# Optimization experiments

Measured on AMD Instinct MI355X. Metric: run time of the kernel, lower is better.

Reference implementation:

```python
import jax, jax.numpy as jnp
import numpy as np

B, S, N, SD = 1024, 8, 64, 36
EPS = 1e-5

def _lrelu(x):
    return jnp.where(x > 0, x, 0.01 * x)

def _inorm(x, g, b):
    # x: [B,S,N,C]; InstanceNorm(axis=3) on a [1,1,N,C] tensor normalizes over N per channel
    mu = jnp.mean(x, axis=2, keepdims=True)
    var = jnp.var(x, axis=2, keepdims=True)
    return (x - mu) * jax.lax.rsqrt(var + EPS) * g + b

def _conv1d_same(x, w, b):
    # x: [B,S,Cin], w: [K,Cin,Cout]; TF 'same' even-kernel pads (0, k-1-pl)
    k = w.shape[0]
    pl = (k - 1) // 2
    y = jax.lax.conv_general_dilated(x, w, (1,), [(pl, k - 1 - pl)],
                                     dimension_numbers=('NWC', 'WIO', 'NWC'))
    return y + b

def setup_inputs() -> dict:
    key = jax.random.key(0)
    ks = iter(jax.random.split(key, 64))
    d = {}
    d['fts'] = jax.random.normal(next(ks), (B, S, N, 5), jnp.float32)
    d['state'] = jax.random.normal(next(ks), (B, S, SD), jnp.float32)
    def w(shape, scale=0.05):
        return jax.random.normal(next(ks), shape, jnp.float32) * scale
    # pointnet (1x1 Conv2D == pointwise matmul)
    d['pw1'] = w((5, 32)); d['pb1'] = jnp.zeros((32,)); d['pg1'] = jnp.ones((32,)); d['pbe1'] = jnp.zeros((32,))
    d['pw2'] = w((32, 64)); d['pb2'] = jnp.zeros((64,)); d['pg2'] = jnp.ones((64,)); d['pbe2'] = jnp.zeros((64,))
    d['pw3'] = w((64, 128)); d['pb3'] = jnp.zeros((128,)); d['pg3'] = jnp.ones((128,)); d['pbe3'] = jnp.zeros((128,))
    d['pw4'] = w((128, 128)); d['pb4'] = jnp.zeros((128,))
    # fts_mergenet Conv1D stack + Dense
    d['mw1'] = w((2, 128, 128)); d['mb1'] = jnp.zeros((128,))
    d['mw2'] = w((2, 128, 64)); d['mb2'] = jnp.zeros((64,))
    d['mw3'] = w((2, 64, 64)); d['mb3'] = jnp.zeros((64,))
    d['mw4'] = w((2, 64, 64)); d['mb4'] = jnp.zeros((64,))
    d['mdw'] = w((S * 64, 128)); d['mdb'] = jnp.zeros((128,))
    # states_conv Conv1D stack + Dense
    d['sw1'] = w((2, SD, 128)); d['sb1'] = jnp.zeros((128,))
    d['sw2'] = w((2, 128, 64)); d['sb2'] = jnp.zeros((64,))
    d['sw3'] = w((2, 64, 64)); d['sb3'] = jnp.zeros((64,))
    d['sw4'] = w((2, 64, 64)); d['sb4'] = jnp.zeros((64,))
    d['sdw'] = w((S * 64, 128)); d['sdb'] = jnp.zeros((128,))
    # control module Dense stack
    d['cw1'] = w((256, 128)); d['cb1'] = jnp.zeros((128,))
    d['cw2'] = w((128, 64)); d['cb2'] = jnp.zeros((64,))
    d['cw3'] = w((64, 32)); d['cb3'] = jnp.zeros((32,))
    d['cw4'] = w((32, 4)); d['cb4'] = jnp.zeros((4,))
    return d

def reference(fts, state, pw1, pb1, pg1, pbe1, pw2, pb2, pg2, pbe2,
              pw3, pb3, pg3, pbe3, pw4, pb4,
              mw1, mb1, mw2, mb2, mw3, mb3, mw4, mb4, mdw, mdb,
              sw1, sb1, sw2, sb2, sw3, sb3, sw4, sb4, sdw, sdb,
              cw1, cb1, cw2, cb2, cw3, cb3, cw4, cb4):
    # --- pointnet, fully batched over (B,S) instead of tf.map_fn per timestep ---
    x = fts  # [B,S,N,5]
    x = _lrelu(_inorm(jnp.einsum('bsnc,cd->bsnd', x, pw1) + pb1, pg1, pbe1))
    x = _lrelu(_inorm(jnp.einsum('bsnc,cd->bsnd', x, pw2) + pb2, pg2, pbe2))
    x = _lrelu(_inorm(jnp.einsum('bsnc,cd->bsnd', x, pw3) + pb3, pg3, pbe3))
    x = jnp.einsum('bsnc,cd->bsnd', x, pw4) + pb4
    emb = jnp.mean(x, axis=2)  # GlobalAveragePooling2D over (1,N) -> [B,S,128]
    # --- fts_mergenet ---
    y = _lrelu(_conv1d_same(emb, mw1, mb1))
    y = _lrelu(_conv1d_same(y, mw2, mb2))
    y = _lrelu(_conv1d_same(y, mw3, mb3))
    y = _lrelu(_conv1d_same(y, mw4, mb4))
    fts_emb = y.reshape(y.shape[0], -1) @ mdw + mdb  # [B,128]
    # --- states branch ---
    z = _lrelu(_conv1d_same(state, sw1, sb1))
    z = _lrelu(_conv1d_same(z, sw2, sb2))
    z = _lrelu(_conv1d_same(z, sw3, sb3))
    z = _conv1d_same(z, sw4, sb4)  # no activation after 4th conv
    st_emb = z.reshape(z.shape[0], -1) @ sdw + sdb  # [B,128]
    # --- control head ---
    t = jnp.concatenate([fts_emb, st_emb], axis=1)  # [B,256]
    t = _lrelu(t @ cw1 + cb1)
    t = _lrelu(t @ cw2 + cb2)
    t = _lrelu(t @ cw3 + cb3)
    out = t @ cw4 + cb4  # [B,4]
    thrust = jax.nn.sigmoid(out[:, :1])
    body = jnp.tanh(out[:, 1:])
    mult = jnp.array([21.0, 6.0, 6.0, 6.0], dtype=out.dtype)
    return jnp.concatenate([thrust, body], axis=1) * mult
```

## Files before the change

### kernel.cpp

```cpp
#include <hip/hip_runtime.h>
#include <math.h>

#define THREADS 256

constexpr int S   = 8;
constexpr int NPT = 64;
constexpr int SD  = 36;
constexpr float EPS = 1e-5f;

typedef float v4f __attribute__((ext_vector_type(4)));
typedef __attribute__((ext_vector_type(8))) short bf8;
typedef __attribute__((ext_vector_type(4))) float f4;

__device__ __forceinline__ float lrelu(float x) { return x > 0.f ? x : 0.01f * x; }

__device__ __forceinline__ unsigned short f2bf(float x) {
  union { float f; unsigned u; } v; v.f = x;
  unsigned r = v.u + 0x7FFFu + ((v.u >> 16) & 1u);
  return (unsigned short)(r >> 16);
}

__device__ __forceinline__ void pack_frag(const float* __restrict__ src, unsigned short* __restrict__ dst,
                                          int slot, int NT, int TS, int CIN, int N) {
  const int f = slot >> 6, l = slot & 63;
  const int nt = f % NT, kt = f / NT;
  const int n = nt * 16 + (l & 15), g = (l >> 4);
  unsigned short* d = dst + (size_t)f * 512 + l * 8;
#pragma unroll
  for (int j = 0; j < 8; ++j) {
    int k = kt * 32 + g * 8 + j;
    float v;
    if (TS > 0) { int tap = k / TS, c = k - tap * TS; v = (c < CIN) ? src[(tap * CIN + c) * N + n] : 0.f; }
    else        v = (CIN == 0 || k < CIN) ? src[k * N + n] : 0.f;
    d[j] = f2bf(v);
  }
}

#define WOFF_PNW1 0
#define WOFF_PNW2 1024
#define WOFF_PNW3 3072
#define WOFF_MW1  11264
#define WOFF_MW2  44032
#define WOFF_MW3  60416
#define WOFF_MW4  68608
#define WOFF_MDW  76800
#define WOFF_SW1  142336
#define WOFF_SW2  154624
#define WOFF_SW3  171008
#define WOFF_SW4  179200
#define WOFF_SDW  187392

__global__ __launch_bounds__(THREADS)
void fold_kernel(const float* __restrict__ pw4, const float* __restrict__ pb4,
                 const float* __restrict__ mw1, const float* __restrict__ mb1,
                 float* __restrict__ w1f, float* __restrict__ mb1p, float* __restrict__ mb1p7) {
  const int t = threadIdx.x, bid = blockIdx.x;
  if (bid < 256) {
    const int tap = bid >> 7, c = bid & 127;
    __shared__ float row[128];
    __shared__ float part[256];
    if (t < 128) row[t] = pw4[c * 128 + t];
    __syncthreads();
    const int n = t & 127, h = t >> 7;
    float a = 0.f;
#pragma unroll 8
    for (int d = h * 64; d < h * 64 + 64; ++d)
      a = fmaf(row[d], mw1[((size_t)tap * 128 + d) * 128 + n], a);
    part[t] = a;
    __syncthreads();
    if (t < 128) w1f[((size_t)tap * 128 + c) * 128 + t] = part[t] + part[128 + t];
  } else if (bid == 256) {
    if (t < 128) {
      float a = mb1[t];
#pragma unroll 8
      for (int k = 0; k < 128; ++k)
        a = fmaf(pb4[k], mw1[(size_t)k * 128 + t] + mw1[(size_t)(128 + k) * 128 + t], a);
      mb1p[t] = a;
    }
  } else {
    if (t < 128) {
      float a = mb1[t];
#pragma unroll 8
      for (int k = 0; k < 128; ++k) a = fmaf(pb4[k], mw1[(size_t)k * 128 + t], a);
      mb1p7[t] = a;
    }
  }
}

__global__ void prep_weights(const float* __restrict__ pw1, const float* __restrict__ pw2,
    const float* __restrict__ pw3, const float* __restrict__ w1fold,
    const float* __restrict__ mw2, const float* __restrict__ mw3,
    const float* __restrict__ mw4, const float* __restrict__ mdw,
    const float* __restrict__ sw1, const float* __restrict__ sw2, const float* __restrict__ sw3,
    const float* __restrict__ sw4, const float* __restrict__ sdw,
    unsigned short* __restrict__ wf) {
  const int slot = blockIdx.x * 256 + threadIdx.x;
  if      (slot <   128) pack_frag(pw1,    wf + WOFF_PNW1, slot,          2,   0,   5,  32);
  else if (slot <   384) pack_frag(pw2,    wf + WOFF_PNW2, slot - 128,    4,   0,   0,  64);
  else if (slot <  1408) pack_frag(pw3,    wf + WOFF_PNW3, slot - 384,    8,   0,   0, 128);
  else if (slot <  5504) pack_frag(w1fold, wf + WOFF_MW1,  slot - 1408,   8, 128, 128, 128);
  else if (slot <  7552) pack_frag(mw2,    wf + WOFF_MW2,  slot - 5504,   4, 128, 128,  64);
  else if (slot <  8576) pack_frag(mw3,    wf + WOFF_MW3,  slot - 7552,   4,  64,  64,  64);
  else if (slot <  9600) pack_frag(mw4,    wf + WOFF_MW4,  slot - 8576,   4,  64,  64,  64);
  else if (slot < 17792) pack_frag(mdw,    wf + WOFF_MDW,  slot - 9600,   8,   0,   0, 128);
  else if (slot < 19328) pack_frag(sw1,    wf + WOFF_SW1,  slot - 17792,  8,  48,  36, 128);
  else if (slot < 21376) pack_frag(sw2,    wf + WOFF_SW2,  slot - 19328,  4, 128, 128,  64);
  else if (slot < 22400) pack_frag(sw3,    wf + WOFF_SW3,  slot - 21376,  4,  64,  64,  64);
  else if (slot < 23424) pack_frag(sw4,    wf + WOFF_SW4,  slot - 22400,  4,  64,  64,  64);
  else if (slot < 31616) pack_frag(sdw,    wf + WOFF_SDW,  slot - 23424,  8,   0,   0, 128);
}

__global__ __launch_bounds__(THREADS)
void pointnet_kernel(const float* __restrict__ fts,
    const unsigned short* __restrict__ w1f, const float* __restrict__ pg1, const float* __restrict__ pbe1,
    const unsigned short* __restrict__ w2f, const float* __restrict__ pg2, const float* __restrict__ pbe2,
    const unsigned short* __restrict__ w3f, const float* __restrict__ pg3, const float* __restrict__ pbe3,
    unsigned short* __restrict__ xbar_out)
{
  const int p = blockIdx.x;
  const int t = threadIdx.x;
  const int l = t & 63, w = t >> 6;
  const int g = l >> 4, lc = l & 15;

  __shared__ unsigned short xinb[64 * 40];
  __shared__ unsigned short x1b[64 * 40];
  __shared__ unsigned short x2b[64 * 72];

  {
    const float* src = fts + (size_t)p * 320;
    unsigned* xz = (unsigned*)xinb;
    for (int i = t; i < 1280; i += THREADS) {
      int row = i / 20, cp = i % 20;
      int c0 = 2 * cp;
      unsigned short lo = (c0 < 5) ? f2bf(src[row * 5 + c0]) : (unsigned short)0;
      unsigned short hi = (c0 + 1 < 5) ? f2bf(src[row * 5 + c0 + 1]) : (unsigned short)0;
      xz[i] = (unsigned)lo | ((unsigned)hi << 16);
    }
  }
  __syncthreads();

  if (w < 2) {
    f4 c1[4];
#pragma unroll
    for (int mt = 0; mt < 4; ++mt) c1[mt] = f4{0.f, 0.f, 0.f, 0.f};
    bf8 bfrag = *(const bf8*)(w1f + ((size_t)w * 64 + l) * 8);
#pragma unroll
    for (int mt = 0; mt < 4; ++mt) {
      bf8 afrag = *(const bf8*)(xinb + (mt * 16 + lc) * 40 + g * 8);
      c1[mt] = __builtin_amdgcn_mfma_f32_16x16x32_bf16(afrag, bfrag, c1[mt], 0, 0, 0);
    }
    float s = 0.f, q = 0.f;
#pragma unroll
    for (int mt = 0; mt < 4; ++mt)
#pragma unroll
      for (int r = 0; r < 4; ++r) { float v = c1[mt][r]; s += v; q = fmaf(v, v, q); }
    s += __shfl_xor(s, 16, 64); s += __shfl_xor(s, 32, 64);
    q += __shfl_xor(q, 16, 64); q += __shfl_xor(q, 32, 64);
    const int ch = w * 16 + lc;
    float mu  = s * (1.f / NPT);
    float inv = rsqrtf(q * (1.f / NPT) - mu * mu + EPS);
    float a = inv * pg1[ch];
    float bb = fmaf(-mu, a, pbe1[ch]);
#pragma unroll
    for (int mt = 0; mt < 4; ++mt)
#pragma unroll
      for (int r = 0; r < 4; ++r) {
        int row = mt * 16 + g * 4 + r;
        x1b[row * 40 + ch] = f2bf(lrelu(fmaf(c1[mt][r], a, bb)));
      }
  }
  __syncthreads();

  f4 c2[4];
#pragma unroll
  for (int mt = 0; mt < 4; ++mt) c2[mt] = f4{0.f, 0.f, 0.f, 0.f};
  {
    bf8 bfrag = *(const bf8*)(w2f + ((size_t)w * 64 + l) * 8);
#pragma unroll
    for (int mt = 0; mt < 4; ++mt) {
      bf8 afrag = *(const bf8*)(x1b + (mt * 16 + lc) * 40 + g * 8);
      c2[mt] = __builtin_amdgcn_mfma_f32_16x16x32_bf16(afrag, bfrag, c2[mt], 0, 0, 0);
    }
  }
  {
    float s = 0.f, q = 0.f;
#pragma unroll
    for (int mt = 0; mt < 4; ++mt)
#pragma unroll
      for (int r = 0; r < 4; ++r) { float v = c2[mt][r]; s += v; q = fmaf(v, v, q); }
    s += __shfl_xor(s, 16, 64); s += __shfl_xor(s, 32, 64);
    q += __shfl_xor(q, 16, 64); q += __shfl_xor(q, 32, 64);
    const int ch = w * 16 + lc;
    float mu  = s * (1.f / NPT);
    float inv = rsqrtf(q * (1.f / NPT) - mu * mu + EPS);
    float a = inv * pg2[ch];
    float bb = fmaf(-mu, a, pbe2[ch]);
#pragma unroll
    for (int mt = 0; mt < 4; ++mt)
#pragma unroll
      for (int r = 0; r < 4; ++r) {
        int row = mt * 16 + g * 4 + r;
        x2b[row * 72 + ch] = f2bf(lrelu(fmaf(c2[mt][r], a, bb)));
      }
  }
  __syncthreads();

  f4 c3[4][2];
#pragma unroll
  for (int mt = 0; mt < 4; ++mt)
#pragma unroll
    for (int n = 0; n < 2; ++n) c3[mt][n] = f4{0.f, 0.f, 0.f, 0.f};
  bf8 bf3[2][2];
#pragma unroll
  for (int ntl = 0; ntl < 2; ++ntl)
#pragma unroll
    for (int kt = 0; kt < 2; ++kt)
      bf3[ntl][kt] = *(const bf8*)(w3f + ((size_t)(kt * 8 + (2 * w + ntl)) * 64 + l) * 8);
#pragma unroll
  for (int mt = 0; mt < 4; ++mt)
#pragma unroll
    for (int kt = 0; kt < 2; ++kt) {
      bf8 afrag = *(const bf8*)(x2b + (mt * 16 + lc) * 72 + kt * 32 + g * 8);
#pragma unroll
      for (int ntl = 0; ntl < 2; ++ntl)
        c3[mt][ntl] = __builtin_amdgcn_mfma_f32_16x16x32_bf16(afrag, bf3[ntl][kt], c3[mt][ntl], 0, 0, 0);
    }

#pragma unroll
  for (int ntl = 0; ntl < 2; ++ntl) {
    float s = 0.f, q = 0.f;
#pragma unroll
    for (int mt = 0; mt < 4; ++mt)
#pragma unroll
      for (int r = 0; r < 4; ++r) { float v = c3[mt][ntl][r]; s += v; q = fmaf(v, v, q); }
    s += __shfl_xor(s, 16, 64); s += __shfl_xor(s, 32, 64);
    q += __shfl_xor(q, 16, 64); q += __shfl_xor(q, 32, 64);
    const int ch = w * 32 + ntl * 16 + lc;
    float mu  = s * (1.f / NPT);
    float inv = rsqrtf(q * (1.f / NPT) - mu * mu + EPS);
    float a = inv * pg3[ch];
    float bb = fmaf(-mu, a, pbe3[ch]);
    float m = 0.f;
#pragma unroll
    for (int mt = 0; mt < 4; ++mt)
#pragma unroll
      for (int r = 0; r < 4; ++r) m += lrelu(fmaf(c3[mt][ntl][r], a, bb));
    m += __shfl_xor(m, 16, 64); m += __shfl_xor(m, 32, 64);
    if (g == 0) xbar_out[(size_t)p * 128 + ch] = f2bf(m * (1.f / NPT));
  }
}

template<int KT, int NT, int TS, int SPI, int SPO, bool ACT>
__device__ __forceinline__ void mfma_conv(const unsigned short* __restrict__ xin,
    unsigned short* __restrict__ xout, const unsigned short* __restrict__ wfr,
    const float* __restrict__ bias, const float* __restrict__ bias7, int w, int l) {
  const int g = l >> 4, lc = l & 15;
  const int arow = w * 16 + lc, abl = arow >> 3, an = arow & 7;
  f4 acc[NT];
#pragma unroll
  for (int nt = 0; nt < NT; ++nt) acc[nt] = f4{0.f, 0.f, 0.f, 0.f};
#pragma unroll
  for (int kt = 0; kt < KT; ++kt) {
    const int k0 = kt * 32 + g * 8;
    const int tap = k0 / TS, c = k0 - tap * TS;
    bf8 a = *(const bf8*)(xin + (abl * 9 + an + tap) * SPI + c);
#pragma unroll
    for (int nt = 0; nt < NT; ++nt) {
      bf8 b = *(const bf8*)(wfr + ((size_t)(kt * NT + nt) * 64 + l) * 8);
      acc[nt] = __builtin_amdgcn_mfma_f32_16x16x32_bf16(a, b, acc[nt], 0, 0, 0);
    }
  }
  const int orow0 = w * 16 + g * 4;
#pragma unroll
  for (int nt = 0; nt < NT; ++nt) {
    const float bv  = bias[nt * 16 + lc];
    const float bv7 = bias7[nt * 16 + lc];
#pragma unroll
    for (int r = 0; r < 4; ++r) {
      const int rr = orow0 + r, obl = rr >> 3, on = rr & 7;
      float v = acc[nt][r] + (on == 7 ? bv7 : bv);
      if (ACT) v = lrelu(v);
      xout[(obl * 9 + on) * SPO + nt * 16 + lc] = f2bf(v);
    }
  }
}

__device__ __forceinline__ void mfma_dense512(const unsigned short* __restrict__ xin,
    float* __restrict__ P, const unsigned short* __restrict__ wfr, int w, int l) {
  const int g = l >> 4, lc = l & 15;
  const int bl = lc & 7;
  f4 acc[8];
#pragma unroll
  for (int nt = 0; nt < 8; ++nt) acc[nt] = f4{0.f, 0.f, 0.f, 0.f};
#pragma unroll
  for (int kt2 = 0; kt2 < 4; ++kt2) {
    const int kt = w * 4 + kt2;
    const int k0 = kt * 32 + g * 8;
    const int n = k0 >> 6, c = k0 & 63;
    bf8 a = *(const bf8*)(xin + (bl * 9 + n) * 72 + c);
#pragma unroll
    for (int nt = 0; nt < 8; ++nt) {
      bf8 b = *(const bf8*)(wfr + ((size_t)(kt * 8 + nt) * 64 + l) * 8);
      acc[nt] = __builtin_amdgcn_mfma_f32_16x16x32_bf16(a, b, acc[nt], 0, 0, 0);
    }
  }
  if (g < 2) {
#pragma unroll
    for (int nt = 0; nt < 8; ++nt)
#pragma unroll
      for (int r = 0; r < 4; ++r) {
        const int rr = g * 4 + r;
        P[(w * 8 + rr) * 128 + nt * 16 + lc] = acc[nt][r];
      }
  }
}

__global__ __launch_bounds__(THREADS)
void tail_mfma_kernel(const unsigned short* __restrict__ xbar, const float* __restrict__ state,
    const unsigned short* __restrict__ wf,
    const float* __restrict__ mb1p, const float* __restrict__ mb1p7,
    const float* __restrict__ mb2, const float* __restrict__ mb3,
    const float* __restrict__ mb4, const float* __restrict__ mdb,
    const float* __restrict__ sb1, const float* __restrict__ sb2, const float* __restrict__ sb3,
    const float* __restrict__ sb4, const float* __restrict__ sdb,
    float* __restrict__ femb, float* __restrict__ semb)
{
  const int t = threadIdx.x, l = t & 63, w = t >> 6;
  const bool merge = blockIdx.x < 128;
  const int bg = merge ? blockIdx.x : blockIdx.x - 128;

  __shared__ unsigned short lds[24768];
  unsigned short* BufX = lds;
  unsigned short* BufY = lds + 9792;
  unsigned short* BufZ = lds + 19584;

  { unsigned* z = (unsigned*)BufX; for (int i = t; i < 4896; i += THREADS) z[i] = 0; }
  for (int i = t; i < 8 * 136; i += THREADS) BufY[((i / 136) * 9 + 8) * 136 + (i % 136)] = 0;
  for (int i = t; i < 8 * 72;  i += THREADS) BufZ[((i / 72)  * 9 + 8) * 72  + (i % 72)]  = 0;

  if (merge) {
    for (int i = t; i < 1024; i += THREADS) {
      int bl = i >> 7, rem = i & 127, n = rem >> 4, sl = rem & 15;
      bf8 v = *(const bf8*)(xbar + (size_t)((bg * 8 + bl) * 8 + n) * 128 + sl * 8);
      *(bf8*)(BufX + (bl * 9 + n) * 136 + sl * 8) = v;
    }
  } else {
    for (int i = t; i < 2304; i += THREADS) {
      int bl = i / 288, rem = i % 288, n = rem / 36, c = rem % 36;
      BufX[(bl * 9 + n) * 48 + c] = f2bf(state[((size_t)(bg * 8 + bl) * 8 + n) * 36 + c]);
    }
  }
  __syncthreads();

  if (merge) mfma_conv<8, 8, 128, 136, 136, true>(BufX, BufY, wf + WOFF_MW1, mb1p, mb1p7, w, l);
  else       mfma_conv<3, 8,  48,  48, 136, true>(BufX, BufY, wf + WOFF_SW1, sb1, sb1, w, l);
  __syncthreads();
  if (merge) mfma_conv<8, 4, 128, 136, 72, true>(BufY, BufZ, wf + WOFF_MW2, mb2, mb2, w, l);
  else       mfma_conv<8, 4, 128, 136, 72, true>(BufY, BufZ, wf + WOFF_SW2, sb2, sb2, w, l);
  __syncthreads();
  for (int i = t; i < 8 * 72; i += THREADS) BufX[((i / 72) * 9 + 8) * 72 + (i % 72)] = 0;
  __syncthreads();
  if (merge) mfma_conv<4, 4, 64, 72, 72, true>(BufZ, BufX, wf + WOFF_MW3, mb3, mb3, w, l);
  else       mfma_conv<4, 4, 64, 72, 72, true>(BufZ, BufX, wf + WOFF_SW3, sb3, sb3, w, l);
  __syncthreads();
  if (merge) mfma_conv<4, 4, 64, 72, 72, true >(BufX, BufY, wf + WOFF_MW4, mb4, mb4, w, l);
  else       mfma_conv<4, 4, 64, 72, 72, false>(BufX, BufY, wf + WOFF_SW4, sb4, sb4, w, l);
  __syncthreads();

  float* P = (float*)lds;
  mfma_dense512(BufY, P, wf + (merge ? WOFF_MDW : WOFF_SDW), w, l);
  __syncthreads();

  const float* bias = merge ? mdb : sdb;
  float* outg = (merge ? femb : semb) + (size_t)bg * 1024;
  for (int i = t; i < 1024; i += THREADS) {
    int ch = i & 127, b = i >> 7;
    outg[i] = bias[ch] + P[(0 * 8 + b) * 128 + ch] + P[(1 * 8 + b) * 128 + ch]
                       + P[(2 * 8 + b) * 128 + ch] + P[(3 * 8 + b) * 128 + ch];
  }
}

template<int CIN, int COUT, bool ACT>
__device__ __forceinline__ void wave_dense(const float* __restrict__ in, float* __restrict__ out,
                                           const float* __restrict__ W, const float* __restrict__ bias, int l) {
  if constexpr (COUT >= 64) {
    constexpr int NC = COUT / 64;
    const int d0 = l * NC;
    float acc[NC];
#pragma unroll
    for (int k = 0; k < NC; ++k) acc[k] = bias[d0 + k];
#pragma unroll 4
    for (int c4 = 0; c4 < CIN / 4; ++c4) {
      v4f x4 = *(const v4f*)(in + 4 * c4);
#pragma unroll
      for (int j = 0; j < 4; ++j) {
        const float* wr = W + (4 * c4 + j) * COUT + d0;
#pragma unroll
        for (int k = 0; k < NC; ++k) acc[k] = fmaf(x4[j], wr[k], acc[k]);
      }
    }
#pragma unroll
    for (int k = 0; k < NC; ++k) out[d0 + k] = ACT ? lrelu(acc[k]) : acc[k];
  } else {
    if (l < COUT) {
      float acc = bias[l];
#pragma unroll 4
      for (int c4 = 0; c4 < CIN / 4; ++c4) {
        v4f x4 = *(const v4f*)(in + 4 * c4);
#pragma unroll
        for (int j = 0; j < 4; ++j) acc = fmaf(x4[j], W[(4 * c4 + j) * COUT + l], acc);
      }
      out[l] = ACT ? lrelu(acc) : acc;
    }
  }
}

__global__ __launch_bounds__(THREADS)
void head_kernel(const float* __restrict__ femb, const float* __restrict__ semb,
    const float* __restrict__ cw1, const float* __restrict__ cb1,
    const float* __restrict__ cw2, const float* __restrict__ cb2,
    const float* __restrict__ cw3, const float* __restrict__ cb3,
    const float* __restrict__ cw4, const float* __restrict__ cb4,
    float* __restrict__ out)
{
  const int t = threadIdx.x, l = t & 63, w = t >> 6;
  const int b = blockIdx.x * 4 + w;
  __shared__ float cat[4][256];
  __shared__ float hb[4][232];

  cat[w][l]       = femb[(size_t)b * 128 + l];
  cat[w][64 + l]  = femb[(size_t)b * 128 + 64 + l];
  cat[w][128 + l] = semb[(size_t)b * 128 + l];
  cat[w][192 + l] = semb[(size_t)b * 128 + 64 + l];
  __syncthreads();
  wave_dense<256, 128, true>(cat[w], hb[w], cw1, cb1, l);
  __syncthreads();
  wave_dense<128, 64, true>(hb[w], hb[w] + 128, cw2, cb2, l);
  __syncthreads();
  wave_dense<64, 32, true>(hb[w] + 128, hb[w] + 192, cw3, cb3, l);
  __syncthreads();
  if (l < 4) {
    float acc = cb4[l];
#pragma unroll
    for (int c = 0; c < 32; ++c) acc = fmaf(hb[w][192 + c], cw4[c * 4 + l], acc);
    out[(size_t)b * 4 + l] = (l == 0) ? 21.f / (1.f + expf(-acc)) : 6.f * tanhf(acc);
  }
}

extern "C" void kernel_launch(void* const* d_in, const int* in_sizes, int n_in,
                              void* d_out, int out_size, void* d_ws, size_t ws_size,
                              hipStream_t stream) {
  const float* p[44];
  for (int i = 0; i < 44; ++i) p[i] = (const float*)d_in[i];

  unsigned short* xbar_bf = (unsigned short*)d_ws;
  float* femb  = (float*)((char*)d_ws + 2097152);
  float* w1fld = (float*)((char*)d_ws + 2097152);
  float* semb  = (float*)((char*)d_ws + 2621440);
  unsigned short* wf = (unsigned short*)((char*)d_ws + 3145728);
  float* mb1p  = (float*)((char*)d_ws + 3651584);
  float* mb1p7 = (float*)((char*)d_ws + 3652096);

  fold_kernel<<<258, THREADS, 0, stream>>>(p[14], p[15], p[16], p[17], w1fld, mb1p, mb1p7);

  prep_weights<<<124, THREADS, 0, stream>>>(
      p[2], p[6], p[10], w1fld,
      p[18], p[20], p[22], p[24],
      p[26], p[28], p[30], p[32], p[34],
      wf);

  pointnet_kernel<<<1024 * S, THREADS, 0, stream>>>(
      p[0],
      wf + WOFF_PNW1, p[4], p[5],
      wf + WOFF_PNW2, p[8], p[9],
      wf + WOFF_PNW3, p[12], p[13],
      xbar_bf);

  tail_mfma_kernel<<<256, THREADS, 0, stream>>>(
      xbar_bf, p[1], wf,
      mb1p, mb1p7, p[19], p[21], p[23], p[25],
      p[27], p[29], p[31], p[33], p[35],
      femb, semb);

  head_kernel<<<256, THREADS, 0, stream>>>(
      femb, semb,
      p[36], p[37], p[38], p[39], p[40], p[41], p[42], p[43],
      (float*)d_out);
}
```

Measured before the change: 83.35 us.

## Fuse weight folding into prep kernel and simplify input staging and conversions

Removes the separate fold_kernel launch by computing the pw4·mw1 folded weights directly inside prep_weights, writing bf16 MFMA fragments without an fp32 intermediate, and computing the folded biases in extra prep threads. The pointnet input staging loop is replaced with a single pass per thread (row = t>>2) that writes zero padding directly. lrelu becomes fmaxf and bf16 conversion uses the library intrinsic. The fused fold does 128-step serial dot products per thread in the prep kernel, which may lengthen that kernel's critical path in exchange for one fewer launch.

```diff
diff --git a/kernel.cpp b/kernel.cpp
--- a/kernel.cpp
+++ b/kernel.cpp
@@ -1,4 +1,5 @@
 #include <hip/hip_runtime.h>
+#include <hip/hip_bf16.h>
 #include <math.h>
 
 #define THREADS 256
@@ -12,12 +13,10 @@
 typedef __attribute__((ext_vector_type(8))) short bf8;
 typedef __attribute__((ext_vector_type(4))) float f4;
 
-__device__ __forceinline__ float lrelu(float x) { return x > 0.f ? x : 0.01f * x; }
+__device__ __forceinline__ float lrelu(float x) { return fmaxf(x, 0.01f * x); }
 
 __device__ __forceinline__ unsigned short f2bf(float x) {
-  union { float f; unsigned u; } v; v.f = x;
-  unsigned r = v.u + 0x7FFFu + ((v.u >> 16) & 1u);
-  return (unsigned short)(r >> 16);
+  return __builtin_bit_cast(unsigned short, __float2bfloat16(x));
 }
 
 __device__ __forceinline__ void pack_frag(const float* __restrict__ src, unsigned short* __restrict__ dst,
@@ -34,6 +33,26 @@
     else        v = (CIN == 0 || k < CIN) ? src[k * N + n] : 0.f;
     d[j] = f2bf(v);
   }
+}
+
+__device__ __forceinline__ void pack_frag_fold(const float* __restrict__ pw4,
+    const float* __restrict__ mw1, unsigned short* __restrict__ dst, int slot) {
+  const int f = slot >> 6, l = slot & 63;
+  const int nt = f & 7, kt = f >> 3;
+  const int n = nt * 16 + (l & 15), g = l >> 4;
+  const int k0 = kt * 32 + g * 8;
+  const int tap = k0 >> 7, c0 = k0 & 127;
+  float acc[8] = {};
+  const float* mcol = mw1 + (size_t)tap * 128 * 128 + n;
+  const float* pr   = pw4 + (size_t)c0 * 128;
+  for (int d = 0; d < 128; ++d) {
+    float m = mcol[(size_t)d * 128];
+#pragma unroll
+    for (int j = 0; j < 8; ++j) acc[j] = fmaf(pr[j * 128 + d], m, acc[j]);
+  }
+  unsigned short* dd = dst + (size_t)f * 512 + l * 8;
+#pragma unroll
+  for (int j = 0; j < 8; ++j) dd[j] = f2bf(acc[j]);
 }
 
 #define WOFF_PNW1 0
@@ -50,55 +69,20 @@
 #define WOFF_SW4  179200
 #define WOFF_SDW  187392
 
-__global__ __launch_bounds__(THREADS)
-void fold_kernel(const float* __restrict__ pw4, const float* __restrict__ pb4,
-                 const float* __restrict__ mw1, const float* __restrict__ mb1,
-                 float* __restrict__ w1f, float* __restrict__ mb1p, float* __restrict__ mb1p7) {
-  const int t = threadIdx.x, bid = blockIdx.x;
-  if (bid < 256) {
-    const int tap = bid >> 7, c = bid & 127;
-    __shared__ float row[128];
-    __shared__ float part[256];
-    if (t < 128) row[t] = pw4[c * 128 + t];
-    __syncthreads();
-    const int n = t & 127, h = t >> 7;
-    float a = 0.f;
-#pragma unroll 8
-    for (int d = h * 64; d < h * 64 + 64; ++d)
-      a = fmaf(row[d], mw1[((size_t)tap * 128 + d) * 128 + n], a);
-    part[t] = a;
-    __syncthreads();
-    if (t < 128) w1f[((size_t)tap * 128 + c) * 128 + t] = part[t] + part[128 + t];
-  } else if (bid == 256) {
-    if (t < 128) {
-      float a = mb1[t];
-#pragma unroll 8
-      for (int k = 0; k < 128; ++k)
-        a = fmaf(pb4[k], mw1[(size_t)k * 128 + t] + mw1[(size_t)(128 + k) * 128 + t], a);
-      mb1p[t] = a;
-    }
-  } else {
-    if (t < 128) {
-      float a = mb1[t];
-#pragma unroll 8
-      for (int k = 0; k < 128; ++k) a = fmaf(pb4[k], mw1[(size_t)k * 128 + t], a);
-      mb1p7[t] = a;
-    }
-  }
-}
-
 __global__ void prep_weights(const float* __restrict__ pw1, const float* __restrict__ pw2,
-    const float* __restrict__ pw3, const float* __restrict__ w1fold,
+    const float* __restrict__ pw3,
+    const float* __restrict__ pw4, const float* __restrict__ pb4,
+    const float* __restrict__ mw1, const float* __restrict__ mb1,
     const float* __restrict__ mw2, const float* __restrict__ mw3,
     const float* __restrict__ mw4, const float* __restrict__ mdw,
     const float* __restrict__ sw1, const float* __restrict__ sw2, const float* __restrict__ sw3,
     const float* __restrict__ sw4, const float* __restrict__ sdw,
-    unsigned short* __restrict__ wf) {
+    unsigned short* __restrict__ wf, float* __restrict__ mb1p, float* __restrict__ mb1p7) {
   const int slot = blockIdx.x * 256 + threadIdx.x;
   if      (slot <   128) pack_frag(pw1,    wf + WOFF_PNW1, slot,          2,   0,   5,  32);
   else if (slot <   384) pack_frag(pw2,    wf + WOFF_PNW2, slot - 128,    4,   0,   0,  64);
   else if (slot <  1408) pack_frag(pw3,    wf + WOFF_PNW3, slot - 384,    8,   0,   0, 128);
-  else if (slot <  5504) pack_frag(w1fold, wf + WOFF_MW1,  slot - 1408,   8, 128, 128, 128);
+  else if (slot <  5504) pack_frag_fold(pw4, mw1, wf + WOFF_MW1, slot - 1408);
   else if (slot <  7552) pack_frag(mw2,    wf + WOFF_MW2,  slot - 5504,   4, 128, 128,  64);
   else if (slot <  8576) pack_frag(mw3,    wf + WOFF_MW3,  slot - 7552,   4,  64,  64,  64);
   else if (slot <  9600) pack_frag(mw4,    wf + WOFF_MW4,  slot - 8576,   4,  64,  64,  64);
@@ -108,6 +92,18 @@
   else if (slot < 22400) pack_frag(sw3,    wf + WOFF_SW3,  slot - 21376,  4,  64,  64,  64);
   else if (slot < 23424) pack_frag(sw4,    wf + WOFF_SW4,  slot - 22400,  4,  64,  64,  64);
   else if (slot < 31616) pack_frag(sdw,    wf + WOFF_SDW,  slot - 23424,  8,   0,   0, 128);
+  else if (slot < 31744) {
+    const int n = slot - 31616;
+    float a = mb1[n];
+    for (int d = 0; d < 128; ++d)
+      a = fmaf(pb4[d], mw1[(size_t)d * 128 + n] + mw1[(size_t)(128 + d) * 128 + n], a);
+    mb1p[n] = a;
+  } else if (slot < 31872) {
+    const int n = slot - 31744;
+    float a = mb1[n];
+    for (int d = 0; d < 128; ++d) a = fmaf(pb4[d], mw1[(size_t)d * 128 + n], a);
+    mb1p7[n] = a;
+  }
 }
 
 __global__ __launch_bounds__(THREADS)
@@ -129,13 +125,17 @@
   {
     const float* src = fts + (size_t)p * 320;
     unsigned* xz = (unsigned*)xinb;
-    for (int i = t; i < 1280; i += THREADS) {
-      int row = i / 20, cp = i % 20;
-      int c0 = 2 * cp;
-      unsigned short lo = (c0 < 5) ? f2bf(src[row * 5 + c0]) : (unsigned short)0;
-      unsigned short hi = (c0 + 1 < 5) ? f2bf(src[row * 5 + c0 + 1]) : (unsigned short)0;
-      xz[i] = (unsigned)lo | ((unsigned)hi << 16);
-    }
+    const int row = t >> 2, cp = t & 3;
+    const float* sr = src + row * 5;
+    unsigned v0 = 0u;
+    if (cp == 0)      v0 = (unsigned)f2bf(sr[0]) | ((unsigned)f2bf(sr[1]) << 16);
+    else if (cp == 1) v0 = (unsigned)f2bf(sr[2]) | ((unsigned)f2bf(sr[3]) << 16);
+    else if (cp == 2) v0 = (unsigned)f2bf(sr[4]);
+    unsigned* xr = xz + row * 20;
+    xr[cp]      = v0;
+    xr[cp + 4]  = 0u;
+    xr[cp + 8]  = 0u;
+    xr[cp + 12] = 0u;
   }
   __syncthreads();
 
@@ -455,19 +455,17 @@
 
   unsigned short* xbar_bf = (unsigned short*)d_ws;
   float* femb  = (float*)((char*)d_ws + 2097152);
-  float* w1fld = (float*)((char*)d_ws + 2097152);
   float* semb  = (float*)((char*)d_ws + 2621440);
   unsigned short* wf = (unsigned short*)((char*)d_ws + 3145728);
   float* mb1p  = (float*)((char*)d_ws + 3651584);
   float* mb1p7 = (float*)((char*)d_ws + 3652096);
 
-  fold_kernel<<<258, THREADS, 0, stream>>>(p[14], p[15], p[16], p[17], w1fld, mb1p, mb1p7);
-
-  prep_weights<<<124, THREADS, 0, stream>>>(
-      p[2], p[6], p[10], w1fld,
+  prep_weights<<<125, THREADS, 0, stream>>>(
+      p[2], p[6], p[10],
+      p[14], p[15], p[16], p[17],
       p[18], p[20], p[22], p[24],
       p[26], p[28], p[30], p[32], p[34],
-      wf);
+      wf, mb1p, mb1p7);
 
   pointnet_kernel<<<1024 * S, THREADS, 0, stream>>>(
       p[0],
```

Measured after the change: 79.26 us. 4.9% less time.
